# Kernel optimization log

Hardware: AMD Instinct MI355X
Metric: run time of the kernel (lower is better)

The kernel has to match this reference:

```python
import jax, jax.numpy as jnp
import numpy as np

N_NODES = 100_000
N_EDGES = 1_600_000
IN_C, HID_C, OUT_C = 128, 64, 32


def gcn_conv(x, W, b, src, dst, n_nodes):
    """PyG GCNConv with add_self_loops=True, symmetric normalization.
    out = D^{-1/2} (A + I) D^{-1/2} (x @ W) + b, with D = deg(A) + 1.
    Self-loop contribution added analytically to avoid materializing loop edges."""
    h = x @ W                                            # [N, F_out]
    deg = jnp.zeros((n_nodes,), h.dtype).at[dst].add(1.0) + 1.0
    dinv = jax.lax.rsqrt(deg)                            # deg >= 1 from self-loops
    norm = dinv[src] * dinv[dst]                         # [E]
    agg = jnp.zeros_like(h).at[dst].add(h[src] * norm[:, None])
    agg = agg + h * (dinv * dinv)[:, None]               # self-loop term
    return agg + b


def setup_inputs() -> dict:
    key = jax.random.key(0)
    ks = jax.random.split(key, 9)
    x = jax.random.normal(ks[0], (N_NODES, IN_C), dtype=jnp.float32)
    edge_index = jax.random.randint(ks[1], (2, N_EDGES), 0, N_NODES, dtype=jnp.int64)
    g = lambda k, fi, fo: jax.random.normal(k, (fi, fo), jnp.float32) * np.sqrt(2.0 / (fi + fo)).astype(np.float32)
    W1 = g(ks[2], IN_C, HID_C)
    b1 = jnp.zeros((HID_C,), jnp.float32)
    W2 = g(ks[3], HID_C, OUT_C)
    b2 = jnp.zeros((OUT_C,), jnp.float32)
    Wl = g(ks[4], IN_C + HID_C + OUT_C, OUT_C)
    bl = jnp.zeros((OUT_C,), jnp.float32)
    return {"x": x, "edge_index": edge_index, "W1": W1, "b1": b1,
            "W2": W2, "b2": b2, "Wl": Wl, "bl": bl}


def reference(x, edge_index, W1, b1, W2, b2, Wl, bl):
    src, dst = edge_index[0], edge_index[1]
    n = x.shape[0]
    h1 = jax.nn.relu(gcn_conv(x, W1, b1, src, dst, n))   # dropout is identity in eval
    h2 = gcn_conv(h1, W2, b2, src, dst, n)
    cat = jnp.concatenate([x, h1, h2], axis=1)           # [N, in+hid+out]
    return jax.nn.log_softmax(cat @ Wl + bl, axis=-1)
```

## Files before the change

kernel.cpp:

```cpp
#include <hip/hip_runtime.h>
#include <hip/hip_bf16.h>
#include <hip/hip_fp16.h>

typedef __hip_bfloat16 bf16;
typedef __attribute__((ext_vector_type(8))) short short8;
typedef __attribute__((ext_vector_type(4))) float f32x4;

#define MFMA16(a, b, c) __builtin_amdgcn_mfma_f32_16x16x32_bf16((a), (b), (c), 0, 0, 0)

static __device__ __forceinline__ float ldf(const void* p, long long i, bool f32) {
    return f32 ? ((const float*)p)[i] : __bfloat162float(((const bf16*)p)[i]);
}

static __device__ __forceinline__ short f2bs(float v) {
    union { bf16 h; short s; } u; u.h = __float2bfloat16(v); return u.s;
}

static __device__ __forceinline__ unsigned int pack_bf16x2(float a, float b) {
    return (unsigned int)(unsigned short)f2bs(a) | ((unsigned int)(unsigned short)f2bs(b) << 16);
}

__global__ __launch_bounds__(256, 4)
void sniff_kernel(const void* __restrict__ x, const void* __restrict__ w,
                  const int* __restrict__ ei, int E, int* __restrict__ flags) {
    __shared__ int cnt;
    if (threadIdx.x == 0) cnt = 0;
    __syncthreads();
    if (blockIdx.x < 2) {
        const unsigned short* u = (const unsigned short*)(blockIdx.x == 0 ? x : w);
        int bad = 0;
        for (int i = threadIdx.x; i < 4096; i += 256) {
            unsigned e = (u[i] >> 7) & 0xFF;
            if (e >= 0xA0) bad++;
        }
        atomicAdd(&cnt, bad);
        __syncthreads();
        if (threadIdx.x == 0) flags[blockIdx.x] = (cnt > 16) ? 1 : 0;
    } else {
        int nz = 0;
        for (int i = threadIdx.x; i < 1024; i += 256)
            if (ei[2 * i + 1] != 0) nz++;
        atomicAdd(&cnt, nz);
        __syncthreads();
        if (threadIdx.x == 0) flags[2] = (cnt == 0) ? 1 : 0;
    }
}

static __device__ __forceinline__ int ld_src(const int* ei, int E, int e, bool i64) {
    return i64 ? ei[2 * e] : ei[e];
}
static __device__ __forceinline__ int ld_dst(const int* ei, int E, int e, bool i64) {
    return i64 ? ei[2 * (E + e)] : ei[E + e];
}


__global__ __launch_bounds__(256, 4)
void bhist_kernel(const int* __restrict__ ei, int E, const int* __restrict__ flags,
                  int shift, int NB, int* __restrict__ bucketCount) {
    __shared__ int h[256];
    for (int i = threadIdx.x; i < 256; i += 256) h[i] = 0;
    __syncthreads();
    bool i64 = flags[2] != 0;
    int base = blockIdx.x * 4096;
    for (int i = 0; i < 16; i++) {
        int e = base + i * 256 + threadIdx.x;
        if (e < E) atomicAdd(&h[ld_dst(ei, E, e, i64) >> shift], 1);
    }
    __syncthreads();
    for (int i = threadIdx.x; i < NB; i += 256)
        if (h[i]) atomicAdd(&bucketCount[i], h[i]);
}

__global__ __launch_bounds__(256, 4)
void bscan_kernel(const int* __restrict__ bucketCount, int NB,
                  int* __restrict__ bucketBase, int* __restrict__ bcursor, int E) {
    __shared__ int bs[256];
    int v = ((int)threadIdx.x < NB) ? bucketCount[threadIdx.x] : 0;
    bs[threadIdx.x] = v;
    __syncthreads();
    for (int off = 1; off < 256; off <<= 1) {
        int t = ((int)threadIdx.x >= off) ? bs[threadIdx.x - off] : 0;
        __syncthreads();
        bs[threadIdx.x] += t;
        __syncthreads();
    }
    int excl = bs[threadIdx.x] - v;
    if ((int)threadIdx.x < NB) { bucketBase[threadIdx.x] = excl; bcursor[threadIdx.x] = excl; }
    if (threadIdx.x == 0) bucketBase[NB] = E;
}

__global__ __launch_bounds__(256, 4)
void bpart_kernel(const int* __restrict__ ei, int E, const int* __restrict__ flags,
                  int shift, int NB, int* __restrict__ bcursor, int2* __restrict__ ebuf) {
    __shared__ int h[256];
    __shared__ int gofs[256];
    __shared__ int2 se[4096];
    for (int i = threadIdx.x; i < 256; i += 256) h[i] = 0;
    __syncthreads();
    bool i64 = flags[2] != 0;
    int base = blockIdx.x * 4096;
    for (int i = 0; i < 16; i++) {
        int e = base + i * 256 + threadIdx.x;
        if (e < E) {
            int s = ld_src(ei, E, e, i64), d = ld_dst(ei, E, e, i64);
            se[i * 256 + threadIdx.x] = make_int2(s, d);
            atomicAdd(&h[d >> shift], 1);
        }
    }
    __syncthreads();
    if ((int)threadIdx.x < NB) {
        int c = h[threadIdx.x];
        gofs[threadIdx.x] = c ? atomicAdd(&bcursor[threadIdx.x], c) : 0;
    }
    __syncthreads();
    for (int i = threadIdx.x; i < 256; i += 256) h[i] = 0;
    __syncthreads();
    for (int i = 0; i < 16; i++) {
        int e = base + i * 256 + threadIdx.x;
        if (e < E) {
            int2 v = se[i * 256 + threadIdx.x];
            int b = v.y >> shift;
            int p = atomicAdd(&h[b], 1);
            ebuf[gofs[b] + p] = v;
        }
    }
}

__global__ __launch_bounds__(256, 2)
void bbuild_kernel(const int2* __restrict__ ebuf, const int* __restrict__ bucketBase,
                   int shift, int N, int E, int* __restrict__ rowptr,
                   float* __restrict__ dinv, int* __restrict__ csr_src) {
    __shared__ int cnt[1024];
    __shared__ int exc[1024];
    __shared__ int bs[256];
    int b = blockIdx.x;
    int nodeBase = b << shift;
    int width = 1 << shift;
    int nn = N - nodeBase; if (nn > width) nn = width;
    int beg = bucketBase[b], end = bucketBase[b + 1];
    for (int i = threadIdx.x; i < width; i += 256) cnt[i] = 0;
    __syncthreads();
    for (int e = beg + threadIdx.x; e < end; e += 256)
        atomicAdd(&cnt[ebuf[e].y - nodeBase], 1);
    __syncthreads();
    int per = width / 256;
    int s = 0;
    int base4 = threadIdx.x * per;
    for (int i = 0; i < per; i++) s += cnt[base4 + i];
    bs[threadIdx.x] = s;
    __syncthreads();
    for (int off = 1; off < 256; off <<= 1) {
        int t = ((int)threadIdx.x >= off) ? bs[threadIdx.x - off] : 0;
        __syncthreads();
        bs[threadIdx.x] += t;
        __syncthreads();
    }
    int run = bs[threadIdx.x] - s;
    for (int i = 0; i < per; i++) { exc[base4 + i] = run; run += cnt[base4 + i]; }
    __syncthreads();
    for (int i = threadIdx.x; i < nn; i += 256) {
        int node = nodeBase + i;
        rowptr[node] = beg + exc[i];
        dinv[node] = rsqrtf((float)cnt[i] + 1.0f);
    }
    __syncthreads();
    for (int i = threadIdx.x; i < width; i += 256) cnt[i] = 0;
    __syncthreads();
    for (int e = beg + threadIdx.x; e < end; e += 256) {
        int2 v = ebuf[e];
        int l = v.y - nodeBase;
        int p = atomicAdd(&cnt[l], 1);
        csr_src[beg + exc[l] + p] = v.x;
    }
    if (b == 0 && threadIdx.x == 0) rowptr[N] = E;
}

__global__ __launch_bounds__(256, 4)
void repack_kernel(const void* __restrict__ W1, const void* __restrict__ W2,
                   const void* __restrict__ Wl, const int* __restrict__ flags,
                   bf16* __restrict__ Bp1, bf16* __restrict__ Bp2, bf16* __restrict__ Bp3) {
    bool fw = flags[1] != 0;
    const void* W; bf16* Bp; int ntiles, nc, nfrag;
    if (blockIdx.x == 0)      { W = W1; Bp = Bp1; ntiles = 4; nc = 64; nfrag = 16; }
    else if (blockIdx.x == 1) { W = W2; Bp = Bp2; ntiles = 2; nc = 32; nfrag = 4;  }
    else                      { W = Wl; Bp = Bp3; ntiles = 2; nc = 32; nfrag = 14; }
    for (int s = threadIdx.x; s < nfrag * 64; s += 256) {
        int f = s >> 6, lane = s & 63;
        int kstep = f / ntiles, ntile = f % ntiles;
        int n = ntile * 16 + (lane & 15);
        int kbase = kstep * 32 + (lane >> 4) * 8;
#pragma unroll
        for (int j = 0; j < 8; j++)
            Bp[s * 8 + j] = __float2bfloat16(ldf(W, (long long)(kbase + j) * nc + n, fw));
    }
}

__global__ __launch_bounds__(256, 4)
void cvt_x_kernel(const void* __restrict__ x, const int* __restrict__ flags,
                  short* __restrict__ xb, long long total8) {
    long long i = (long long)blockIdx.x * 256 + threadIdx.x;
    if (i >= total8) return;
    bool fx = flags[0] != 0;
    short8 o;
    if (fx) {
        const float4* xf = (const float4*)x;
        float4 a = xf[i * 2], b = xf[i * 2 + 1];
        o[0] = f2bs(a.x); o[1] = f2bs(a.y); o[2] = f2bs(a.z); o[3] = f2bs(a.w);
        o[4] = f2bs(b.x); o[5] = f2bs(b.y); o[6] = f2bs(b.z); o[7] = f2bs(b.w);
    } else {
        o = ((const short8*)x)[i];
    }
    ((short8*)xb)[i] = o;
}

__global__ __launch_bounds__(256, 3)
void gemm1_mfma_kernel(const short* __restrict__ xb, const bf16* __restrict__ Bpack,
                       const float* __restrict__ dinv, __half* __restrict__ h1g, int N) {
    int lane = threadIdx.x & 63, wave = threadIdx.x >> 6;
    int m = lane & 15, quad = lane >> 4;
    int base = blockIdx.x * 128 + wave * 32;
    if (base >= N) return;
    const short8* bp = (const short8*)Bpack;
    short8 B[16];
#pragma unroll
    for (int i = 0; i < 16; i++) B[i] = bp[i * 64 + lane];
    if (base + 32 <= N) {
#pragma unroll
        for (int t = 0; t < 2; t++) {
            int r0 = base + t * 16;
            const short* xr = &xb[(long long)(r0 + m) * 128 + quad * 8];
            short8 A[4];
#pragma unroll
            for (int k = 0; k < 4; k++) A[k] = *(const short8*)(xr + k * 32);
            f32x4 acc[4];
#pragma unroll
            for (int nt = 0; nt < 4; nt++) acc[nt] = (f32x4){0.f, 0.f, 0.f, 0.f};
#pragma unroll
            for (int k = 0; k < 4; k++) {
#pragma unroll
                for (int nt = 0; nt < 4; nt++) acc[nt] = MFMA16(A[k], B[k * 4 + nt], acc[nt]);
            }
            float dv[4];
#pragma unroll
            for (int r = 0; r < 4; r++) dv[r] = dinv[r0 + quad * 4 + r];
            __half* o = &h1g[(long long)(r0 + quad * 4) * 64 + m];
#pragma unroll
            for (int nt = 0; nt < 4; nt++) {
#pragma unroll
                for (int r = 0; r < 4; r++) o[(long long)r * 64 + nt * 16] = __float2half(acc[nt][r] * dv[r]);
            }
        }
    } else {
#pragma unroll
        for (int t = 0; t < 2; t++) {
            int r0 = base + t * 16;
            int row = r0 + m;
            short8 A[4];
#pragma unroll
            for (int k = 0; k < 4; k++) A[k] = (short8){0,0,0,0,0,0,0,0};
            if (row < N) {
                const short* xr = &xb[(long long)row * 128 + quad * 8];
#pragma unroll
                for (int k = 0; k < 4; k++) A[k] = *(const short8*)(xr + k * 32);
            }
            f32x4 acc[4];
#pragma unroll
            for (int nt = 0; nt < 4; nt++) acc[nt] = (f32x4){0.f, 0.f, 0.f, 0.f};
#pragma unroll
            for (int k = 0; k < 4; k++) {
#pragma unroll
                for (int nt = 0; nt < 4; nt++) acc[nt] = MFMA16(A[k], B[k * 4 + nt], acc[nt]);
            }
#pragma unroll
            for (int r = 0; r < 4; r++) {
                int orow = r0 + quad * 4 + r;
                if (orow < N) {
                    float dv = dinv[orow];
                    __half* o = &h1g[(long long)orow * 64 + m];
#pragma unroll
                    for (int nt = 0; nt < 4; nt++) o[nt * 16] = __float2half(acc[nt][r] * dv);
                }
            }
        }
    }
}

__global__ __launch_bounds__(256, 8)
void gather1_kernel(const unsigned int* __restrict__ h1g, const float* __restrict__ dinv,
                    const int* __restrict__ rowptr, const int* __restrict__ csr_src,
                    const void* __restrict__ bptr, const int* __restrict__ flags,
                    unsigned int* __restrict__ h1b, int N) {
    bool fw = flags[1] != 0;
    int lane = threadIdx.x & 63;
    int c = lane & 31, hf = lane >> 5;
    int wv = __builtin_amdgcn_readfirstlane(threadIdx.x >> 6);
    int node = blockIdx.x * 4 + wv;
    if (node >= N) return;
    int beg = rowptr[node], end = rowptr[node + 1];
    const unsigned int* hL = h1g + c;
    float a0 = 0.f, a1 = 0.f;
    int p = beg;
    for (; p + 32 <= end; p += 32) {
        unsigned int v[16];
#pragma unroll
        for (int u = 0; u < 16; u++) {
            int s0 = csr_src[p + 2 * u];
            int s1 = csr_src[p + 2 * u + 1];
            int s = hf ? s1 : s0;
            v[u] = hL[(long long)s * 32];
        }
#pragma unroll
        for (int u = 0; u < 16; u++) {
            float2 f = __half22float2(*(const __half2*)&v[u]);
            a0 += f.x; a1 += f.y;
        }
    }
    for (; p + 16 <= end; p += 16) {
        unsigned int v[8];
#pragma unroll
        for (int u = 0; u < 8; u++) {
            int s0 = csr_src[p + 2 * u];
            int s1 = csr_src[p + 2 * u + 1];
            int s = hf ? s1 : s0;
            v[u] = hL[(long long)s * 32];
        }
#pragma unroll
        for (int u = 0; u < 8; u++) {
            float2 f = __half22float2(*(const __half2*)&v[u]);
            a0 += f.x; a1 += f.y;
        }
    }
    if (p < end) {
        unsigned int v[8]; float m[8];
#pragma unroll
        for (int u = 0; u < 8; u++) {
            int i0 = p + 2 * u, i1 = i0 + 1;
            int s0 = csr_src[(i0 < end) ? i0 : beg];
            int s1 = csr_src[(i1 < end) ? i1 : beg];
            int s = hf ? s1 : s0;
            m[u] = hf ? ((i1 < end) ? 1.f : 0.f) : ((i0 < end) ? 1.f : 0.f);
            v[u] = hL[(long long)s * 32];
        }
#pragma unroll
        for (int u = 0; u < 8; u++) {
            float2 f = __half22float2(*(const __half2*)&v[u]);
            a0 = fmaf(f.x, m[u], a0);
            a1 = fmaf(f.y, m[u], a1);
        }
    }
    a0 += __shfl_xor(a0, 32);
    a1 += __shfl_xor(a1, 32);
    if (hf == 0) {
        unsigned int gsv = h1g[(long long)node * 32 + c];
        float2 gs = __half22float2(*(const __half2*)&gsv);
        float dvd = dinv[node];
        float o0 = dvd * (a0 + gs.x) + ldf(bptr, 2 * c, fw);
        float o1 = dvd * (a1 + gs.y) + ldf(bptr, 2 * c + 1, fw);
        h1b[(long long)node * 32 + c] = pack_bf16x2(fmaxf(o0, 0.f), fmaxf(o1, 0.f));
    }
}

__global__ __launch_bounds__(256, 4)
void gemm2_mfma_kernel(const short* __restrict__ h1b, const bf16* __restrict__ Bpack,
                       const float* __restrict__ dinv, __half* __restrict__ h2g, int N) {
    int lane = threadIdx.x & 63, wave = threadIdx.x >> 6;
    int m = lane & 15, quad = lane >> 4;
    int r0 = blockIdx.x * 64 + wave * 16;
    if (r0 >= N) return;
    const short8* bp = (const short8*)Bpack;
    short8 B[4];
#pragma unroll
    for (int i = 0; i < 4; i++) B[i] = bp[i * 64 + lane];
    f32x4 acc0 = {0.f,0.f,0.f,0.f}, acc1 = {0.f,0.f,0.f,0.f};
    if (r0 + 16 <= N) {
        const short* xr = &h1b[(long long)(r0 + m) * 64 + quad * 8];
#pragma unroll
        for (int k = 0; k < 2; k++) {
            short8 A = *(const short8*)(xr + k * 32);
            acc0 = MFMA16(A, B[k * 2 + 0], acc0);
            acc1 = MFMA16(A, B[k * 2 + 1], acc1);
        }
        float dv[4];
#pragma unroll
        for (int r = 0; r < 4; r++) dv[r] = dinv[r0 + quad * 4 + r];
        __half* o = &h2g[(long long)(r0 + quad * 4) * 32 + m];
#pragma unroll
        for (int r = 0; r < 4; r++) {
            o[(long long)r * 32]      = __float2half(acc0[r] * dv[r]);
            o[(long long)r * 32 + 16] = __float2half(acc1[r] * dv[r]);
        }
    } else {
        int row = r0 + m;
#pragma unroll
        for (int k = 0; k < 2; k++) {
            short8 A = {0,0,0,0,0,0,0,0};
            if (row < N) A = *(const short8*)&h1b[(long long)row * 64 + k * 32 + quad * 8];
            acc0 = MFMA16(A, B[k * 2 + 0], acc0);
            acc1 = MFMA16(A, B[k * 2 + 1], acc1);
        }
#pragma unroll
        for (int r = 0; r < 4; r++) {
            int orow = r0 + quad * 4 + r;
            if (orow < N) {
                float dv = dinv[orow];
                h2g[(long long)orow * 32 + m]      = __float2half(acc0[r] * dv);
                h2g[(long long)orow * 32 + 16 + m] = __float2half(acc1[r] * dv);
            }
        }
    }
}

__global__ __launch_bounds__(256, 8)
void gather2_kernel(const unsigned int* __restrict__ h2g, const float* __restrict__ dinv,
                    const int* __restrict__ rowptr, const int* __restrict__ csr_src,
                    const void* __restrict__ bptr, const int* __restrict__ flags,
                    unsigned int* __restrict__ h2b, int N) {
    bool fw = flags[1] != 0;
    int lane = threadIdx.x & 63;
    int c = lane & 15, sub = lane >> 4;
    int wv = __builtin_amdgcn_readfirstlane(threadIdx.x >> 6);
    int node = blockIdx.x * 4 + wv;
    if (node >= N) return;
    int beg = rowptr[node], end = rowptr[node + 1];
    const unsigned int* hL = h2g + c;
    float a0 = 0.f, a1 = 0.f;
    int p = beg;
    for (; p + 32 <= end; p += 32) {
        unsigned int v[8];
#pragma unroll
        for (int u = 0; u < 8; u++) {
            int i0 = p + 4 * u;
            int sa0 = csr_src[i0], sa1 = csr_src[i0 + 1];
            int sa2 = csr_src[i0 + 2], sa3 = csr_src[i0 + 3];
            int sA = (sub & 1) ? sa1 : sa0;
            int sB = (sub & 1) ? sa3 : sa2;
            int s  = (sub & 2) ? sB : sA;
            v[u] = hL[(long long)s * 16];
        }
#pragma unroll
        for (int u = 0; u < 8; u++) {
            float2 f = __half22float2(*(const __half2*)&v[u]);
            a0 += f.x; a1 += f.y;
        }
    }
    for (; p + 16 <= end; p += 16) {
        unsigned int v[4];
#pragma unroll
        for (int u = 0; u < 4; u++) {
            int i0 = p + 4 * u;
            int sa0 = csr_src[i0], sa1 = csr_src[i0 + 1];
            int sa2 = csr_src[i0 + 2], sa3 = csr_src[i0 + 3];
            int sA = (sub & 1) ? sa1 : sa0;
            int sB = (sub & 1) ? sa3 : sa2;
            int s  = (sub & 2) ? sB : sA;
            v[u] = hL[(long long)s * 16];
        }
#pragma unroll
        for (int u = 0; u < 4; u++) {
            float2 f = __half22float2(*(const __half2*)&v[u]);
            a0 += f.x; a1 += f.y;
        }
    }
    if (p < end) {
        unsigned int v[4]; float m[4];
#pragma unroll
        for (int u = 0; u < 4; u++) {
            int i0 = p + 4 * u;
            int sa0 = csr_src[(i0     < end) ? i0     : beg];
            int sa1 = csr_src[(i0 + 1 < end) ? i0 + 1 : beg];
            int sa2 = csr_src[(i0 + 2 < end) ? i0 + 2 : beg];
            int sa3 = csr_src[(i0 + 3 < end) ? i0 + 3 : beg];
            int sA = (sub & 1) ? sa1 : sa0;
            int sB = (sub & 1) ? sa3 : sa2;
            int s  = (sub & 2) ? sB : sA;
            float ma = (sub & 1) ? ((i0 + 1 < end) ? 1.f : 0.f) : ((i0 < end) ? 1.f : 0.f);
            float mb = (sub & 1) ? ((i0 + 3 < end) ? 1.f : 0.f) : ((i0 + 2 < end) ? 1.f : 0.f);
            m[u] = (sub & 2) ? mb : ma;
            v[u] = hL[(long long)s * 16];
        }
#pragma unroll
        for (int u = 0; u < 4; u++) {
            float2 f = __half22float2(*(const __half2*)&v[u]);
            a0 = fmaf(f.x, m[u], a0);
            a1 = fmaf(f.y, m[u], a1);
        }
    }
    a0 += __shfl_xor(a0, 16); a1 += __shfl_xor(a1, 16);
    a0 += __shfl_xor(a0, 32); a1 += __shfl_xor(a1, 32);
    if (sub == 0) {
        unsigned int gsv = h2g[(long long)node * 16 + c];
        float2 gs = __half22float2(*(const __half2*)&gsv);
        float dvd = dinv[node];
        float o0 = dvd * (a0 + gs.x) + ldf(bptr, 2 * c, fw);
        float o1 = dvd * (a1 + gs.y) + ldf(bptr, 2 * c + 1, fw);
        h2b[(long long)node * 16 + c] = pack_bf16x2(o0, o1);
    }
}

__global__ __launch_bounds__(256, 2)
void final_mfma_kernel(const short* __restrict__ xb, const short* __restrict__ h1b,
                       const short* __restrict__ h2b, const bf16* __restrict__ Bpack,
                       const void* __restrict__ bl, const int* __restrict__ flags,
                       void* __restrict__ out, int N) {
    bool fw = flags[1] != 0, fx = flags[0] != 0;
    int lane = threadIdx.x & 63, wave = threadIdx.x >> 6;
    int m = lane & 15, quad = lane >> 4;
    int r0 = blockIdx.x * 64 + wave * 16;
    if (r0 >= N) return;
    const short8* bp = (const short8*)Bpack;
    short8 B[14];
#pragma unroll
    for (int i = 0; i < 14; i++) B[i] = bp[i * 64 + lane];
    f32x4 acc0 = {0.f,0.f,0.f,0.f}, acc1 = {0.f,0.f,0.f,0.f};
    bool full = (r0 + 16 <= N);
    int row = r0 + m;
    bool rowok = full || (row < N);
#pragma unroll
    for (int s = 0; s < 7; s++) {
        short8 A = {0,0,0,0,0,0,0,0};
        if (rowok) {
            const short* p;
            if (s < 4)      p = &xb [(long long)row * 128 + s * 32 + quad * 8];
            else if (s < 6) p = &h1b[(long long)row * 64 + (s - 4) * 32 + quad * 8];
            else            p = &h2b[(long long)row * 32 + quad * 8];
            A = *(const short8*)p;
        }
        acc0 = MFMA16(A, B[s * 2 + 0], acc0);
        acc1 = MFMA16(A, B[s * 2 + 1], acc1);
    }
    float bl0 = ldf(bl, m, fw), bl1 = ldf(bl, m + 16, fw);
#pragma unroll
    for (int r = 0; r < 4; r++) {
        float v0 = acc0[r] + bl0, v1 = acc1[r] + bl1;
        float mx = fmaxf(v0, v1);
#pragma unroll
        for (int o = 8; o > 0; o >>= 1) mx = fmaxf(mx, __shfl_xor(mx, o));
        float sm = __expf(v0 - mx) + __expf(v1 - mx);
#pragma unroll
        for (int o = 8; o > 0; o >>= 1) sm += __shfl_xor(sm, o);
        float lse = mx + __logf(sm);
        int orow = r0 + quad * 4 + r;
        if (orow < N) {
            if (fx) {
                ((float*)out)[(long long)orow * 32 + m]      = v0 - lse;
                ((float*)out)[(long long)orow * 32 + 16 + m] = v1 - lse;
            } else {
                ((bf16*)out)[(long long)orow * 32 + m]      = __float2bfloat16(v0 - lse);
                ((bf16*)out)[(long long)orow * 32 + 16 + m] = __float2bfloat16(v1 - lse);
            }
        }
    }
}

extern "C" void kernel_launch(void* const* d_in, const int* in_sizes, int n_in,
                              void* d_out, int out_size, void* d_ws, size_t ws_size,
                              hipStream_t stream) {
    const void* x  = d_in[0];
    const int*  ei = (const int*)d_in[1];
    const void* W1 = d_in[2];
    const void* b1 = d_in[3];
    const void* W2 = d_in[4];
    const void* b2 = d_in[5];
    const void* Wl = d_in[6];
    const void* bl = d_in[7];

    int N = in_sizes[0] / 128;
    int E = in_sizes[1] / 2;

    int shift = 9;
    while (((N + (1 << shift) - 1) >> shift) > 256 && shift < 10) shift++;
    int NB = (N + (1 << shift) - 1) >> shift;

    int* ip      = (int*)d_ws;
    int* flags   = ip;
    int* bucketCount = ip + 16;
    int* bucketBase  = bucketCount + 256;
    int* bcursor     = bucketBase + 272;
    float* dinv  = (float*)(bcursor + 256);
    int* rowptr  = (int*)(dinv + N);
    bf16* Bp1    = (bf16*)(rowptr + N + 16);
    bf16* Bp2    = (bf16*)((int*)Bp1 + 4096);
    bf16* Bp3    = (bf16*)((int*)Bp2 + 1024);
    int* csr_src = (int*)Bp3 + 3584;
    short* xb    = (short*)(csr_src + E);
    int*   Ai    = (int*)xb + (size_t)N * 64;
    int2*  ebuf  = (int2*)Ai;
    __half* h1g  = (__half*)Ai;
    __half* h2g  = (__half*)Ai;
    unsigned int* h2b = (unsigned int*)(Ai + (size_t)N * 48);
    unsigned int* h1b = (unsigned int*)(Ai + (size_t)N * 64);

    hipMemsetAsync(ip, 0, (16 + 256) * sizeof(int), stream);

    sniff_kernel<<<3, 256, 0, stream>>>(x, W1, ei, E, flags);

    int nchunk = (E + 4095) / 4096;
    bhist_kernel<<<nchunk, 256, 0, stream>>>(ei, E, flags, shift, NB, bucketCount);
    bscan_kernel<<<1, 256, 0, stream>>>(bucketCount, NB, bucketBase, bcursor, E);
    bpart_kernel<<<nchunk, 256, 0, stream>>>(ei, E, flags, shift, NB, bcursor, ebuf);
    bbuild_kernel<<<NB, 256, 0, stream>>>(ebuf, bucketBase, shift, N, E, rowptr, dinv, csr_src);

    repack_kernel<<<3, 256, 0, stream>>>(W1, W2, Wl, flags, Bp1, Bp2, Bp3);

    long long total8 = (long long)N * 16;
    cvt_x_kernel<<<(int)((total8 + 255) / 256), 256, 0, stream>>>(x, flags, xb, total8);

    gemm1_mfma_kernel<<<(N + 127) / 128, 256, 0, stream>>>(xb, Bp1, dinv, h1g, N);
    gather1_kernel<<<(N + 3) / 4, 256, 0, stream>>>((const unsigned int*)h1g, dinv, rowptr, csr_src,
                                                    b1, flags, h1b, N);
    gemm2_mfma_kernel<<<(N + 63) / 64, 256, 0, stream>>>((const short*)h1b, Bp2, dinv, h2g, N);
    gather2_kernel<<<(N + 3) / 4, 256, 0, stream>>>((const unsigned int*)h2g, dinv, rowptr, csr_src,
                                                    b2, flags, h2b, N);
    final_mfma_kernel<<<(N + 63) / 64, 256, 0, stream>>>(xb, (const short*)h1b, (const short*)h2b,
                                                         Bp3, bl, flags, d_out, N);
}
```

Baseline: 310.1 us.

## Fuse x conversion into GEMM1 and gather two nodes per wave

Removes the standalone fp32-to-bf16 conversion kernel by converting x inside gemm1 and writing the bf16 copy for the final GEMM from there, which saves one launch and one full read of x. The gather kernels now process two consecutive CSR rows per wave over a merged edge range. Each lane accumulates a total sum and a masked first-node sum, and the second node's sum is recovered by subtraction. This cuts wave-level imbalance and tail waste on short rows, at the cost of extra FMAs, extra masks and possible cancellation error from the subtraction.

```diff
diff --git a/kernel.cpp b/kernel.cpp
--- a/kernel.cpp
+++ b/kernel.cpp
@@ -195,27 +195,11 @@
     }
 }
 
-__global__ __launch_bounds__(256, 4)
-void cvt_x_kernel(const void* __restrict__ x, const int* __restrict__ flags,
-                  short* __restrict__ xb, long long total8) {
-    long long i = (long long)blockIdx.x * 256 + threadIdx.x;
-    if (i >= total8) return;
+__global__ __launch_bounds__(256, 3)
+void gemm1_mfma_kernel(const void* __restrict__ x, const bf16* __restrict__ Bpack,
+                       const float* __restrict__ dinv, const int* __restrict__ flags,
+                       __half* __restrict__ h1g, short* __restrict__ xb, int N) {
     bool fx = flags[0] != 0;
-    short8 o;
-    if (fx) {
-        const float4* xf = (const float4*)x;
-        float4 a = xf[i * 2], b = xf[i * 2 + 1];
-        o[0] = f2bs(a.x); o[1] = f2bs(a.y); o[2] = f2bs(a.z); o[3] = f2bs(a.w);
-        o[4] = f2bs(b.x); o[5] = f2bs(b.y); o[6] = f2bs(b.z); o[7] = f2bs(b.w);
-    } else {
-        o = ((const short8*)x)[i];
-    }
-    ((short8*)xb)[i] = o;
-}
-
-__global__ __launch_bounds__(256, 3)
-void gemm1_mfma_kernel(const short* __restrict__ xb, const bf16* __restrict__ Bpack,
-                       const float* __restrict__ dinv, __half* __restrict__ h1g, int N) {
     int lane = threadIdx.x & 63, wave = threadIdx.x >> 6;
     int m = lane & 15, quad = lane >> 4;
     int base = blockIdx.x * 128 + wave * 32;
@@ -228,10 +212,26 @@
 #pragma unroll
         for (int t = 0; t < 2; t++) {
             int r0 = base + t * 16;
-            const short* xr = &xb[(long long)(r0 + m) * 128 + quad * 8];
             short8 A[4];
-#pragma unroll
-            for (int k = 0; k < 4; k++) A[k] = *(const short8*)(xr + k * 32);
+            if (fx) {
+                const float* xr = &((const float*)x)[(long long)(r0 + m) * 128 + quad * 8];
+#pragma unroll
+                for (int k = 0; k < 4; k++) {
+                    float4 fa = *(const float4*)(xr + k * 32);
+                    float4 fb = *(const float4*)(xr + k * 32 + 4);
+                    short8 o;
+                    o[0] = f2bs(fa.x); o[1] = f2bs(fa.y); o[2] = f2bs(fa.z); o[3] = f2bs(fa.w);
+                    o[4] = f2bs(fb.x); o[5] = f2bs(fb.y); o[6] = f2bs(fb.z); o[7] = f2bs(fb.w);
+                    A[k] = o;
+                }
+                short* xw = &xb[(long long)(r0 + m) * 128 + quad * 8];
+#pragma unroll
+                for (int k = 0; k < 4; k++) *(short8*)(xw + k * 32) = A[k];
+            } else {
+                const short* xr = &((const short*)x)[(long long)(r0 + m) * 128 + quad * 8];
+#pragma unroll
+                for (int k = 0; k < 4; k++) A[k] = *(const short8*)(xr + k * 32);
+            }
             f32x4 acc[4];
 #pragma unroll
             for (int nt = 0; nt < 4; nt++) acc[nt] = (f32x4){0.f, 0.f, 0.f, 0.f};
@@ -259,9 +259,25 @@
 #pragma unroll
             for (int k = 0; k < 4; k++) A[k] = (short8){0,0,0,0,0,0,0,0};
             if (row < N) {
-                const short* xr = &xb[(long long)row * 128 + quad * 8];
-#pragma unroll
-                for (int k = 0; k < 4; k++) A[k] = *(const short8*)(xr + k * 32);
+                if (fx) {
+                    const float* xr = &((const float*)x)[(long long)row * 128 + quad * 8];
+#pragma unroll
+                    for (int k = 0; k < 4; k++) {
+                        float4 fa = *(const float4*)(xr + k * 32);
+                        float4 fb = *(const float4*)(xr + k * 32 + 4);
+                        short8 o;
+                        o[0] = f2bs(fa.x); o[1] = f2bs(fa.y); o[2] = f2bs(fa.z); o[3] = f2bs(fa.w);
+                        o[4] = f2bs(fb.x); o[5] = f2bs(fb.y); o[6] = f2bs(fb.z); o[7] = f2bs(fb.w);
+                        A[k] = o;
+                    }
+                    short* xw = &xb[(long long)row * 128 + quad * 8];
+#pragma unroll
+                    for (int k = 0; k < 4; k++) *(short8*)(xw + k * 32) = A[k];
+                } else {
+                    const short* xr = &((const short*)x)[(long long)row * 128 + quad * 8];
+#pragma unroll
+                    for (int k = 0; k < 4; k++) A[k] = *(const short8*)(xr + k * 32);
+                }
             }
             f32x4 acc[4];
 #pragma unroll
@@ -294,63 +310,80 @@
     int lane = threadIdx.x & 63;
     int c = lane & 31, hf = lane >> 5;
     int wv = __builtin_amdgcn_readfirstlane(threadIdx.x >> 6);
-    int node = blockIdx.x * 4 + wv;
-    if (node >= N) return;
-    int beg = rowptr[node], end = rowptr[node + 1];
+    int n0 = (blockIdx.x * 4 + wv) * 2;
+    if (n0 >= N) return;
+    bool has1 = (n0 + 1 < N);
+    int beg = rowptr[n0];
+    int mid = rowptr[n0 + 1];
+    int end = has1 ? rowptr[n0 + 2] : mid;
     const unsigned int* hL = h1g + c;
-    float a0 = 0.f, a1 = 0.f;
+    float aA0 = 0.f, aA1 = 0.f;
+    float aN0 = 0.f, aN1 = 0.f;
     int p = beg;
     for (; p + 32 <= end; p += 32) {
-        unsigned int v[16];
+        unsigned int v[16]; float r[16];
 #pragma unroll
         for (int u = 0; u < 16; u++) {
             int s0 = csr_src[p + 2 * u];
             int s1 = csr_src[p + 2 * u + 1];
             int s = hf ? s1 : s0;
+            r[u] = ((p + 2 * u + hf) < mid) ? 1.f : 0.f;
             v[u] = hL[(long long)s * 32];
         }
 #pragma unroll
         for (int u = 0; u < 16; u++) {
             float2 f = __half22float2(*(const __half2*)&v[u]);
-            a0 += f.x; a1 += f.y;
+            aA0 += f.x; aA1 += f.y;
+            aN0 = fmaf(f.x, r[u], aN0);
+            aN1 = fmaf(f.y, r[u], aN1);
         }
     }
     for (; p + 16 <= end; p += 16) {
-        unsigned int v[8];
+        unsigned int v[8]; float r[8];
 #pragma unroll
         for (int u = 0; u < 8; u++) {
             int s0 = csr_src[p + 2 * u];
             int s1 = csr_src[p + 2 * u + 1];
             int s = hf ? s1 : s0;
+            r[u] = ((p + 2 * u + hf) < mid) ? 1.f : 0.f;
             v[u] = hL[(long long)s * 32];
         }
 #pragma unroll
         for (int u = 0; u < 8; u++) {
             float2 f = __half22float2(*(const __half2*)&v[u]);
-            a0 += f.x; a1 += f.y;
+            aA0 += f.x; aA1 += f.y;
+            aN0 = fmaf(f.x, r[u], aN0);
+            aN1 = fmaf(f.y, r[u], aN1);
         }
     }
     if (p < end) {
-        unsigned int v[8]; float m[8];
+        unsigned int v[8]; float mk[8], r[8];
 #pragma unroll
         for (int u = 0; u < 8; u++) {
             int i0 = p + 2 * u, i1 = i0 + 1;
             int s0 = csr_src[(i0 < end) ? i0 : beg];
             int s1 = csr_src[(i1 < end) ? i1 : beg];
             int s = hf ? s1 : s0;
-            m[u] = hf ? ((i1 < end) ? 1.f : 0.f) : ((i0 < end) ? 1.f : 0.f);
+            int i = p + 2 * u + hf;
+            mk[u] = (i < end) ? 1.f : 0.f;
+            r[u]  = (i < mid) ? 1.f : 0.f;
             v[u] = hL[(long long)s * 32];
         }
 #pragma unroll
         for (int u = 0; u < 8; u++) {
             float2 f = __half22float2(*(const __half2*)&v[u]);
-            a0 = fmaf(f.x, m[u], a0);
-            a1 = fmaf(f.y, m[u], a1);
-        }
-    }
-    a0 += __shfl_xor(a0, 32);
-    a1 += __shfl_xor(a1, 32);
-    if (hf == 0) {
+            aA0 = fmaf(f.x, mk[u], aA0);
+            aA1 = fmaf(f.y, mk[u], aA1);
+            aN0 = fmaf(f.x, r[u], aN0);
+            aN1 = fmaf(f.y, r[u], aN1);
+        }
+    }
+    aA0 += __shfl_xor(aA0, 32); aA1 += __shfl_xor(aA1, 32);
+    aN0 += __shfl_xor(aN0, 32); aN1 += __shfl_xor(aN1, 32);
+    int node = n0 + hf;
+    if (node < N) {
+        float a0 = hf ? (aA0 - aN0) : aN0;
+        float a1 = hf ? (aA1 - aN1) : aN1;
         unsigned int gsv = h1g[(long long)node * 32 + c];
         float2 gs = __half22float2(*(const __half2*)&gsv);
         float dvd = dinv[node];
@@ -419,14 +452,17 @@
     int lane = threadIdx.x & 63;
     int c = lane & 15, sub = lane >> 4;
     int wv = __builtin_amdgcn_readfirstlane(threadIdx.x >> 6);
-    int node = blockIdx.x * 4 + wv;
-    if (node >= N) return;
-    int beg = rowptr[node], end = rowptr[node + 1];
+    int n0 = (blockIdx.x * 4 + wv) * 2;
+    if (n0 >= N) return;
+    bool has1 = (n0 + 1 < N);
+    int beg = rowptr[n0];
+    int mid = rowptr[n0 + 1];
+    int end = has1 ? rowptr[n0 + 2] : mid;
     const unsigned int* hL = h2g + c;
-    float a0 = 0.f, a1 = 0.f;
+    float aA0 = 0.f, aA1 = 0.f, aN0 = 0.f, aN1 = 0.f;
     int p = beg;
     for (; p + 32 <= end; p += 32) {
-        unsigned int v[8];
+        unsigned int v[8]; float r[8];
 #pragma unroll
         for (int u = 0; u < 8; u++) {
             int i0 = p + 4 * u;
@@ -435,16 +471,19 @@
             int sA = (sub & 1) ? sa1 : sa0;
             int sB = (sub & 1) ? sa3 : sa2;
             int s  = (sub & 2) ? sB : sA;
+            r[u] = ((i0 + sub) < mid) ? 1.f : 0.f;
             v[u] = hL[(long long)s * 16];
         }
 #pragma unroll
         for (int u = 0; u < 8; u++) {
             float2 f = __half22float2(*(const __half2*)&v[u]);
-            a0 += f.x; a1 += f.y;
+            aA0 += f.x; aA1 += f.y;
+            aN0 = fmaf(f.x, r[u], aN0);
+            aN1 = fmaf(f.y, r[u], aN1);
         }
     }
     for (; p + 16 <= end; p += 16) {
-        unsigned int v[4];
+        unsigned int v[4]; float r[4];
 #pragma unroll
         for (int u = 0; u < 4; u++) {
             int i0 = p + 4 * u;
@@ -453,16 +492,19 @@
             int sA = (sub & 1) ? sa1 : sa0;
             int sB = (sub & 1) ? sa3 : sa2;
             int s  = (sub & 2) ? sB : sA;
+            r[u] = ((i0 + sub) < mid) ? 1.f : 0.f;
             v[u] = hL[(long long)s * 16];
         }
 #pragma unroll
         for (int u = 0; u < 4; u++) {
             float2 f = __half22float2(*(const __half2*)&v[u]);
-            a0 += f.x; a1 += f.y;
+            aA0 += f.x; aA1 += f.y;
+            aN0 = fmaf(f.x, r[u], aN0);
+            aN1 = fmaf(f.y, r[u], aN1);
         }
     }
     if (p < end) {
-        unsigned int v[4]; float m[4];
+        unsigned int v[4]; float mk[4], r[4];
 #pragma unroll
         for (int u = 0; u < 4; u++) {
             int i0 = p + 4 * u;
@@ -473,36 +515,47 @@
             int sA = (sub & 1) ? sa1 : sa0;
             int sB = (sub & 1) ? sa3 : sa2;
             int s  = (sub & 2) ? sB : sA;
-            float ma = (sub & 1) ? ((i0 + 1 < end) ? 1.f : 0.f) : ((i0 < end) ? 1.f : 0.f);
-            float mb = (sub & 1) ? ((i0 + 3 < end) ? 1.f : 0.f) : ((i0 + 2 < end) ? 1.f : 0.f);
-            m[u] = (sub & 2) ? mb : ma;
+            int i = i0 + sub;
+            mk[u] = (i < end) ? 1.f : 0.f;
+            r[u]  = (i < mid) ? 1.f : 0.f;
             v[u] = hL[(long long)s * 16];
         }
 #pragma unroll
         for (int u = 0; u < 4; u++) {
             float2 f = __half22float2(*(const __half2*)&v[u]);
-            a0 = fmaf(f.x, m[u], a0);
-            a1 = fmaf(f.y, m[u], a1);
-        }
-    }
-    a0 += __shfl_xor(a0, 16); a1 += __shfl_xor(a1, 16);
-    a0 += __shfl_xor(a0, 32); a1 += __shfl_xor(a1, 32);
-    if (sub == 0) {
-        unsigned int gsv = h2g[(long long)node * 16 + c];
-        float2 gs = __half22float2(*(const __half2*)&gsv);
-        float dvd = dinv[node];
-        float o0 = dvd * (a0 + gs.x) + ldf(bptr, 2 * c, fw);
-        float o1 = dvd * (a1 + gs.y) + ldf(bptr, 2 * c + 1, fw);
-        h2b[(long long)node * 16 + c] = pack_bf16x2(o0, o1);
+            aA0 = fmaf(f.x, mk[u], aA0);
+            aA1 = fmaf(f.y, mk[u], aA1);
+            aN0 = fmaf(f.x, r[u], aN0);
+            aN1 = fmaf(f.y, r[u], aN1);
+        }
+    }
+    aA0 += __shfl_xor(aA0, 16); aA1 += __shfl_xor(aA1, 16);
+    aN0 += __shfl_xor(aN0, 16); aN1 += __shfl_xor(aN1, 16);
+    aA0 += __shfl_xor(aA0, 32); aA1 += __shfl_xor(aA1, 32);
+    aN0 += __shfl_xor(aN0, 32); aN1 += __shfl_xor(aN1, 32);
+    if (sub < 2) {
+        int node = n0 + sub;
+        if (node < N) {
+            float a0 = sub ? (aA0 - aN0) : aN0;
+            float a1 = sub ? (aA1 - aN1) : aN1;
+            unsigned int gsv = h2g[(long long)node * 16 + c];
+            float2 gs = __half22float2(*(const __half2*)&gsv);
+            float dvd = dinv[node];
+            float o0 = dvd * (a0 + gs.x) + ldf(bptr, 2 * c, fw);
+            float o1 = dvd * (a1 + gs.y) + ldf(bptr, 2 * c + 1, fw);
+            h2b[(long long)node * 16 + c] = pack_bf16x2(o0, o1);
+        }
     }
 }
 
 __global__ __launch_bounds__(256, 2)
-void final_mfma_kernel(const short* __restrict__ xb, const short* __restrict__ h1b,
+void final_mfma_kernel(const void* __restrict__ x, const short* __restrict__ xb,
+                       const short* __restrict__ h1b,
                        const short* __restrict__ h2b, const bf16* __restrict__ Bpack,
                        const void* __restrict__ bl, const int* __restrict__ flags,
                        void* __restrict__ out, int N) {
     bool fw = flags[1] != 0, fx = flags[0] != 0;
+    const short* xs = fx ? xb : (const short*)x;
     int lane = threadIdx.x & 63, wave = threadIdx.x >> 6;
     int m = lane & 15, quad = lane >> 4;
     int r0 = blockIdx.x * 64 + wave * 16;
@@ -520,7 +573,7 @@
         short8 A = {0,0,0,0,0,0,0,0};
         if (rowok) {
             const short* p;
-            if (s < 4)      p = &xb [(long long)row * 128 + s * 32 + quad * 8];
+            if (s < 4)      p = &xs [(long long)row * 128 + s * 32 + quad * 8];
             else if (s < 6) p = &h1b[(long long)row * 64 + (s - 4) * 32 + quad * 8];
             else            p = &h2b[(long long)row * 32 + quad * 8];
             A = *(const short8*)p;
@@ -602,15 +655,12 @@
 
     repack_kernel<<<3, 256, 0, stream>>>(W1, W2, Wl, flags, Bp1, Bp2, Bp3);
 
-    long long total8 = (long long)N * 16;
-    cvt_x_kernel<<<(int)((total8 + 255) / 256), 256, 0, stream>>>(x, flags, xb, total8);
-
-    gemm1_mfma_kernel<<<(N + 127) / 128, 256, 0, stream>>>(xb, Bp1, dinv, h1g, N);
-    gather1_kernel<<<(N + 3) / 4, 256, 0, stream>>>((const unsigned int*)h1g, dinv, rowptr, csr_src,
+    gemm1_mfma_kernel<<<(N + 127) / 128, 256, 0, stream>>>(x, Bp1, dinv, flags, h1g, xb, N);
+    gather1_kernel<<<(N + 7) / 8, 256, 0, stream>>>((const unsigned int*)h1g, dinv, rowptr, csr_src,
                                                     b1, flags, h1b, N);
     gemm2_mfma_kernel<<<(N + 63) / 64, 256, 0, stream>>>((const short*)h1b, Bp2, dinv, h2g, N);
-    gather2_kernel<<<(N + 3) / 4, 256, 0, stream>>>((const unsigned int*)h2g, dinv, rowptr, csr_src,
+    gather2_kernel<<<(N + 7) / 8, 256, 0, stream>>>((const unsigned int*)h2g, dinv, rowptr, csr_src,
                                                     b2, flags, h2b, N);
-    final_mfma_kernel<<<(N + 63) / 64, 256, 0, stream>>>(xb, (const short*)h1b, (const short*)h2b,
-                                                         Bp3, bl, flags, d_out, N);
-}
+    final_mfma_kernel<<<(N + 63) / 64, 256, 0, stream>>>(x, (const short*)xb, (const short*)h1b,
+                                                         (const short*)h2b, Bp3, bl, flags, d_out, N);
+}
```

After: 293.2 us. -5.4%, faster.
